# Kernel tuning notes

Hardware: AMD Instinct MI355X
Metric: run time of the kernel (lower is better)

The kernel has to match this reference:

```python
import jax, jax.numpy as jnp
import numpy as np

DIM = 1024
NUM_HEADS = 16
HEAD_DIM = DIM // NUM_HEADS
SCALE = HEAD_DIM ** -0.5
B, N = 2, 2048


def setup_inputs() -> dict:
    key = jax.random.key(0)
    k_x, k_qkv, k_prjw, k_prjb = jax.random.split(key, 4)
    # nn.Linear(dim, 3*dim, bias=False): weight [3*dim, dim]
    s = 1.0 / np.sqrt(DIM)
    return {
        "x": jax.random.normal(k_x, (B, N, DIM), dtype=jnp.float32),
        "w_qkv": jax.random.uniform(k_qkv, (3 * DIM, DIM), jnp.float32, -s, s),
        "w_prj": jax.random.uniform(k_prjw, (DIM, DIM), jnp.float32, -s, s),
        "b_prj": jax.random.uniform(k_prjb, (DIM,), jnp.float32, -s, s),
    }


def reference(x, w_qkv, w_prj, b_prj):
    Bb, Nn, C = x.shape
    qkv = jnp.einsum("bnc,dc->bnd", x, w_qkv)            # [B,N,3C]
    qkv = qkv.reshape(Bb, Nn, 3, NUM_HEADS, HEAD_DIM)
    qkv = jnp.transpose(qkv, (2, 0, 3, 1, 4))            # [3,B,H,N,hd]
    q, k, v = qkv[0], qkv[1], qkv[2]
    attn = jnp.einsum("bhqd,bhkd->bhqk", q, k) * SCALE   # [B,H,N,N]
    attn = jax.nn.softmax(attn, axis=-1)
    out = jnp.einsum("bhqk,bhkd->bhqd", attn, v)         # [B,H,N,hd]
    out = jnp.transpose(out, (0, 2, 1, 3)).reshape(Bb, Nn, C)
    # dropout layers are identity at eval / p=0
    return jnp.einsum("bnc,dc->bnd", out, w_prj) + b_prj
```

## Files before the change

### kernel.cpp

```cpp
#include <hip/hip_runtime.h>

typedef unsigned short u16;
typedef unsigned int u32;
typedef __attribute__((ext_vector_type(8))) short s16x8;
typedef __attribute__((ext_vector_type(4))) short s16x4;
typedef __attribute__((ext_vector_type(4))) float f32x4;

#define DIM    1024
#define NHEADS 16
#define HD     64
#define NSEQ   2048
#define QKVN   3072

__device__ __forceinline__ u16 f2bf(float f) {
  u32 u = __float_as_uint(f);
  u += 0x7FFF + ((u >> 16) & 1);
  return (u16)(u >> 16);
}

__device__ __forceinline__ float vexp2(float x) {
  float r;
  asm volatile("v_exp_f32 %0, %1" : "=v"(r) : "v"(x));
  return r;
}

__device__ __forceinline__ void async16(const u16* g, u16* l) {
  __builtin_amdgcn_global_load_lds(
      (const __attribute__((address_space(1))) unsigned int*)g,
      (__attribute__((address_space(3))) unsigned int*)l, 16, 0, 0);
}

__global__ void cast_all(const float* __restrict__ x, const float* __restrict__ wq,
                         const float* __restrict__ wp, u16* __restrict__ xo,
                         u16* __restrict__ wqo, u16* __restrict__ wpo) {
  int i = blockIdx.x * 256 + threadIdx.x;
  const float4* src; u16* dst; int off;
  if (i < 1048576)      { src = (const float4*)x;  dst = xo;  off = i; }
  else if (i < 1835008) { src = (const float4*)wq; dst = wqo; off = i - 1048576; }
  else                  { src = (const float4*)wp; dst = wpo; off = i - 1835008; }
  float4 f = src[off];
  ushort4 o;
  o.x = f2bf(f.x); o.y = f2bf(f.y); o.z = f2bf(f.z); o.w = f2bf(f.w);
  ((ushort4*)dst)[off] = o;
}

template <bool FINAL>
__global__ __launch_bounds__(256, 3) void gemm_bt(
    const u16* __restrict__ A, const u16* __restrict__ Bw, u16* __restrict__ qkv,
    u16* __restrict__ vt, const float* __restrict__ bias, float* __restrict__ outp) {
  constexpr int K = 1024;
  constexpr int BM = FINAL ? 64 : 128;
  constexpr int MT = FINAL ? 64 : 32;
  constexpr int IT = FINAL ? 2 : 4;
  constexpr int ACALLS = BM / 16;
  constexpr int TCALLS = ACALLS + 8;
  constexpr int PW = TCALLS / 4;
  const int bm = blockIdx.x % MT;
  const int bn = blockIdx.x / MT;
  const int tid = threadIdx.x;
  const int wave = tid >> 6, lane = tid & 63;
  const int q4 = lane >> 4, l15 = lane & 15;
  const int wm = wave >> 1, wn = wave & 1;
  const int m0 = bm * BM, n0 = bn * 128;

  __shared__ alignas(16) u16 lsA[BM * 32];
  __shared__ alignas(16) u16 lsB[128 * 32];

  f32x4 acc[IT][4];
#pragma unroll
  for (int i = 0; i < IT; i++)
#pragma unroll
    for (int j = 0; j < 4; j++) acc[i][j] = (f32x4){0.f, 0.f, 0.f, 0.f};

  for (int k0 = 0; k0 < K; k0 += 32) {
    __syncthreads();
#pragma unroll
    for (int j = 0; j < PW; ++j) {
      int t = wave * PW + j;
      if (t < ACALLS) {
        int lin = t * 64 + lane;
        int r = lin >> 2, c = lin & 3;
        async16(A + (size_t)(m0 + r) * K + k0 + c * 8, lsA + t * 512);
      } else {
        int tb = t - ACALLS;
        int lin = tb * 64 + lane;
        int r = lin >> 2, c = lin & 3;
        async16(Bw + (size_t)(n0 + r) * K + k0 + c * 8, lsB + tb * 512);
      }
    }
    __syncthreads();
    s16x8 af[IT], bfr[4];
#pragma unroll
    for (int i = 0; i < IT; ++i)
      af[i] = *(const s16x8*)(lsA + (wm * (IT * 16) + i * 16 + l15) * 32 + q4 * 8);
#pragma unroll
    for (int j = 0; j < 4; ++j)
      bfr[j] = *(const s16x8*)(lsB + (wn * 64 + j * 16 + l15) * 32 + q4 * 8);
#pragma unroll
    for (int i = 0; i < IT; ++i)
#pragma unroll
      for (int j = 0; j < 4; ++j)
        acc[i][j] = __builtin_amdgcn_mfma_f32_16x16x32_bf16(af[i], bfr[j], acc[i][j], 0, 0, 0);
  }

#pragma unroll
  for (int i = 0; i < IT; i++) {
#pragma unroll
    for (int j = 0; j < 4; j++) {
      int n = n0 + wn * 64 + j * 16 + l15;
      int mb = m0 + wm * (IT * 16) + i * 16 + q4 * 4;
      if (FINAL) {
#pragma unroll
        for (int r = 0; r < 4; r++)
          outp[(size_t)(mb + r) * DIM + n] = acc[i][j][r] + bias[n];
      } else if (n < 2048) {
#pragma unroll
        for (int r = 0; r < 4; r++)
          qkv[(size_t)(mb + r) * QKVN + n] = f2bf(acc[i][j][r]);
      } else {
        int b = mb >> 11, tok = mb & 2047;
        int h = (n >> 6) & 15, hd = n & 63;
        ushort4 pk;
        pk.x = f2bf(acc[i][j][0]); pk.y = f2bf(acc[i][j][1]);
        pk.z = f2bf(acc[i][j][2]); pk.w = f2bf(acc[i][j][3]);
        *(ushort4*)(vt + ((size_t)((b * NHEADS + h) * HD + hd)) * NSEQ + tok) = pk;
      }
    }
  }
}

__global__ __launch_bounds__(256, 2) void attn_kernel(const u16* __restrict__ qkv,
                                                      const u16* __restrict__ vt,
                                                      u16* __restrict__ aout) {
  const int blk = blockIdx.x;
  const int bh = blk & 31, qt = blk >> 5;
  const int b = bh >> 4, h = bh & 15;
  const int tid = threadIdx.x;
  const int wave = tid >> 6, lane = tid & 63;
  const int q4 = lane >> 4, l15 = lane & 15;

  __shared__ alignas(16) u16 lsK[2][64 * 64];
  __shared__ alignas(16) u16 lsV[2][64 * 64];

  const float QSCALE = 0.18033688011112042f;
  s16x8 aq[2][2];
#pragma unroll
  for (int rt = 0; rt < 2; ++rt)
#pragma unroll
    for (int kc = 0; kc < 2; ++kc) {
      int row = b * NSEQ + qt * 128 + wave * 32 + rt * 16 + l15;
      uint4 d = *(const uint4*)(qkv + (size_t)row * QKVN + h * HD + kc * 32 + q4 * 8);
      u32 w[4] = {d.x, d.y, d.z, d.w};
      s16x8 f;
#pragma unroll
      for (int j = 0; j < 8; ++j) {
        u16 u = (u16)(w[j >> 1] >> ((j & 1) * 16));
        float v = __uint_as_float(((u32)u) << 16) * QSCALE;
        f[j] = (short)f2bf(v);
      }
      aq[rt][kc] = f;
    }

  f32x4 o[2][4];
  float lsum[2] = {0.f, 0.f};
#pragma unroll
  for (int rt = 0; rt < 2; ++rt)
#pragma unroll
    for (int ht = 0; ht < 4; ++ht) o[rt][ht] = (f32x4){0.f, 0.f, 0.f, 0.f};

  auto stage = [&](int kt, int buf) {
#pragma unroll
    for (int j = 0; j < 2; ++j) {
      int t = wave * 2 + j;
      int lin = t * 64 + lane;
      int r = lin >> 3, c = (lin & 7) ^ (r & 7);
      async16(qkv + (size_t)(b * NSEQ + kt * 64 + r) * QKVN + DIM + h * HD + c * 8,
              lsK[buf] + t * 512);
      async16(vt + (size_t)(bh * HD + r) * NSEQ + kt * 64 + c * 8,
              lsV[buf] + t * 512);
    }
  };

  stage(0, 0);

  for (int kt = 0; kt < 32; ++kt) {
    const int buf = kt & 1;
    __syncthreads();
    if (kt + 1 < 32) stage(kt + 1, buf ^ 1);

    s16x8 kf[2][4];
#pragma unroll
    for (int kc = 0; kc < 2; ++kc)
#pragma unroll
      for (int ct = 0; ct < 4; ++ct) {
        int r = ct * 16 + l15;
        int c = (kc * 4 + q4) ^ (r & 7);
        kf[kc][ct] = *(const s16x8*)(lsK[buf] + r * 64 + c * 8);
      }
    s16x4 vf[4][4];
#pragma unroll
    for (int ct = 0; ct < 4; ++ct)
#pragma unroll
      for (int ht = 0; ht < 4; ++ht) {
        int row = ht * 16 + l15;
        int g = ct * 2 + (q4 >> 1);
        int p = g ^ (row & 7);
        vf[ct][ht] = *(const s16x4*)(lsV[buf] + row * 64 + p * 8 + (q4 & 1) * 4);
      }

#pragma unroll
    for (int rt = 0; rt < 2; ++rt) {
      f32x4 st[4];
#pragma unroll
      for (int ct = 0; ct < 4; ++ct) st[ct] = (f32x4){0.f, 0.f, 0.f, 0.f};
#pragma unroll
      for (int kc = 0; kc < 2; ++kc)
#pragma unroll
        for (int ct = 0; ct < 4; ++ct)
          st[ct] = __builtin_amdgcn_mfma_f32_16x16x32_bf16(kf[kc][ct], aq[rt][kc], st[ct], 0, 0, 0);

      s16x4 pa[4];
#pragma unroll
      for (int ct = 0; ct < 4; ++ct) {
        u32 u0 = __float_as_uint(vexp2(st[ct][0]));
        u32 u1 = __float_as_uint(vexp2(st[ct][1]));
        u32 u2 = __float_as_uint(vexp2(st[ct][2]));
        u32 u3 = __float_as_uint(vexp2(st[ct][3]));
        lsum[rt] += __uint_as_float(u0 & 0xffff0000u) + __uint_as_float(u1 & 0xffff0000u) +
                    __uint_as_float(u2 & 0xffff0000u) + __uint_as_float(u3 & 0xffff0000u);
        union { u32 w[2]; s16x4 v; } pk;
        pk.w[0] = (u0 >> 16) | (u1 & 0xffff0000u);
        pk.w[1] = (u2 >> 16) | (u3 & 0xffff0000u);
        pa[ct] = pk.v;
      }

#pragma unroll
      for (int ct = 0; ct < 4; ++ct)
#pragma unroll
        for (int ht = 0; ht < 4; ++ht)
          o[rt][ht] = __builtin_amdgcn_mfma_f32_16x16x16bf16_1k(pa[ct], vf[ct][ht], o[rt][ht], 0, 0, 0);
    }
  }

#pragma unroll
  for (int rt = 0; rt < 2; ++rt) {
    lsum[rt] += __shfl_xor(lsum[rt], 16, 64);
    lsum[rt] += __shfl_xor(lsum[rt], 32, 64);
  }

#pragma unroll
  for (int rt = 0; rt < 2; ++rt) {
    float inv[4];
#pragma unroll
    for (int r = 0; r < 4; ++r) inv[r] = 1.0f / __shfl(lsum[rt], q4 * 4 + r, 64);
#pragma unroll
    for (int ht = 0; ht < 4; ++ht)
#pragma unroll
      for (int r = 0; r < 4; ++r) {
        int n = qt * 128 + wave * 32 + rt * 16 + q4 * 4 + r;
        int col = h * HD + ht * 16 + l15;
        aout[(size_t)(b * NSEQ + n) * DIM + col] = f2bf(o[rt][ht][r] * inv[r]);
      }
  }
}

extern "C" void kernel_launch(void* const* d_in, const int* in_sizes, int n_in,
                              void* d_out, int out_size, void* d_ws, size_t ws_size,
                              hipStream_t stream) {
  const float* x     = (const float*)d_in[0];
  const float* w_qkv = (const float*)d_in[1];
  const float* w_prj = (const float*)d_in[2];
  const float* b_prj = (const float*)d_in[3];
  float* out = (float*)d_out;

  char* ws = (char*)d_ws;
  u16* x_bf    = (u16*)(ws);
  u16* wqkv_bf = (u16*)(ws + (size_t)(8u << 20));
  u16* wprj_bf = (u16*)(ws + (size_t)(14u << 20));
  u16* qkv     = (u16*)(ws + (size_t)(16u << 20));
  u16* vt      = (u16*)(ws + (size_t)(40u << 20));
  u16* aout    = (u16*)(ws + (size_t)(48u << 20));

  cast_all<<<8192, 256, 0, stream>>>(x, w_qkv, w_prj, x_bf, wqkv_bf, wprj_bf);
  gemm_bt<false><<<32 * 24, 256, 0, stream>>>(x_bf, wqkv_bf, qkv, vt, nullptr, nullptr);
  attn_kernel<<<512, 256, 0, stream>>>(qkv, vt, aout);
  gemm_bt<true><<<64 * 8, 256, 0, stream>>>(aout, wprj_bf, nullptr, nullptr, b_prj, out);
}
```

Before: 188.0 us.

## Split attention key range across wave groups and merge partial outputs via LDS

The four waves of each attention block are split into two groups. Each group handles half of the key sequence for 64 query rows per wave, so each wave now covers four query tiles instead of two. After the loop, group 1 writes its partial O and row sums to shared memory, and group 0 adds them and normalizes. This raises reuse of each staged K/V tile per wave and halves the loop trip count, at the cost of more registers (doubled accumulators and Q fragments) and an extra LDS reduction at the end. The exp2 inline asm is also replaced by a compiler builtin so the scheduler can see it.

```diff
diff --git a/kernel.cpp b/kernel.cpp
--- a/kernel.cpp
+++ b/kernel.cpp
@@ -19,9 +19,11 @@
 }
 
 __device__ __forceinline__ float vexp2(float x) {
-  float r;
-  asm volatile("v_exp_f32 %0, %1" : "=v"(r) : "v"(x));
-  return r;
+#if __has_builtin(__builtin_amdgcn_exp2f)
+  return __builtin_amdgcn_exp2f(x);
+#else
+  return __expf(x * 0.69314718055994531f);
+#endif
 }
 
 __device__ __forceinline__ void async16(const u16* g, u16* l) {
@@ -137,18 +139,22 @@
   const int b = bh >> 4, h = bh & 15;
   const int tid = threadIdx.x;
   const int wave = tid >> 6, lane = tid & 63;
+  const int g = wave >> 1, wq = wave & 1;
   const int q4 = lane >> 4, l15 = lane & 15;
 
-  __shared__ alignas(16) u16 lsK[2][64 * 64];
-  __shared__ alignas(16) u16 lsV[2][64 * 64];
+  __shared__ alignas(16) u16 smem[32768];
+  u16* lsKb = smem + g * 2 * 4096;
+  u16* lsVb = smem + 16384 + g * 2 * 4096;
+  float* lsO = (float*)smem;
+  float* lsS = lsO + 64 * 132;
 
   const float QSCALE = 0.18033688011112042f;
-  s16x8 aq[2][2];
-#pragma unroll
-  for (int rt = 0; rt < 2; ++rt)
+  s16x8 aq[4][2];
+#pragma unroll
+  for (int rt = 0; rt < 4; ++rt)
 #pragma unroll
     for (int kc = 0; kc < 2; ++kc) {
-      int row = b * NSEQ + qt * 128 + wave * 32 + rt * 16 + l15;
+      int row = b * NSEQ + qt * 128 + wq * 64 + rt * 16 + l15;
       uint4 d = *(const uint4*)(qkv + (size_t)row * QKVN + h * HD + kc * 32 + q4 * 8);
       u32 w[4] = {d.x, d.y, d.z, d.w};
       s16x8 f;
@@ -161,32 +167,35 @@
       aq[rt][kc] = f;
     }
 
-  f32x4 o[2][4];
-  float lsum[2] = {0.f, 0.f};
-#pragma unroll
-  for (int rt = 0; rt < 2; ++rt)
+  f32x4 o[4][4];
+  float lsum[4] = {0.f, 0.f, 0.f, 0.f};
+#pragma unroll
+  for (int rt = 0; rt < 4; ++rt)
 #pragma unroll
     for (int ht = 0; ht < 4; ++ht) o[rt][ht] = (f32x4){0.f, 0.f, 0.f, 0.f};
 
-  auto stage = [&](int kt, int buf) {
-#pragma unroll
-    for (int j = 0; j < 2; ++j) {
-      int t = wave * 2 + j;
+  auto stage = [&](int ktl, int buf) {
+#pragma unroll
+    for (int j = 0; j < 4; ++j) {
+      int t = wq * 4 + j;
       int lin = t * 64 + lane;
       int r = lin >> 3, c = (lin & 7) ^ (r & 7);
-      async16(qkv + (size_t)(b * NSEQ + kt * 64 + r) * QKVN + DIM + h * HD + c * 8,
-              lsK[buf] + t * 512);
-      async16(vt + (size_t)(bh * HD + r) * NSEQ + kt * 64 + c * 8,
-              lsV[buf] + t * 512);
+      int key = g * 1024 + ktl * 64;
+      async16(qkv + (size_t)(b * NSEQ + key + r) * QKVN + DIM + h * HD + c * 8,
+              lsKb + buf * 4096 + t * 512);
+      async16(vt + (size_t)(bh * HD + r) * NSEQ + key + c * 8,
+              lsVb + buf * 4096 + t * 512);
     }
   };
 
   stage(0, 0);
 
-  for (int kt = 0; kt < 32; ++kt) {
+  for (int kt = 0; kt < 16; ++kt) {
     const int buf = kt & 1;
     __syncthreads();
-    if (kt + 1 < 32) stage(kt + 1, buf ^ 1);
+    if (kt + 1 < 16) stage(kt + 1, buf ^ 1);
+    const u16* lsK = lsKb + buf * 4096;
+    const u16* lsV = lsVb + buf * 4096;
 
     s16x8 kf[2][4];
 #pragma unroll
@@ -195,7 +204,7 @@
       for (int ct = 0; ct < 4; ++ct) {
         int r = ct * 16 + l15;
         int c = (kc * 4 + q4) ^ (r & 7);
-        kf[kc][ct] = *(const s16x8*)(lsK[buf] + r * 64 + c * 8);
+        kf[kc][ct] = *(const s16x8*)(lsK + r * 64 + c * 8);
       }
     s16x4 vf[4][4];
 #pragma unroll
@@ -203,13 +212,13 @@
 #pragma unroll
       for (int ht = 0; ht < 4; ++ht) {
         int row = ht * 16 + l15;
-        int g = ct * 2 + (q4 >> 1);
-        int p = g ^ (row & 7);
-        vf[ct][ht] = *(const s16x4*)(lsV[buf] + row * 64 + p * 8 + (q4 & 1) * 4);
-      }
-
-#pragma unroll
-    for (int rt = 0; rt < 2; ++rt) {
+        int gch = ct * 2 + (q4 >> 1);
+        int p = gch ^ (row & 7);
+        vf[ct][ht] = *(const s16x4*)(lsV + row * 64 + p * 8 + (q4 & 1) * 4);
+      }
+
+#pragma unroll
+    for (int rt = 0; rt < 4; ++rt) {
       f32x4 st[4];
 #pragma unroll
       for (int ct = 0; ct < 4; ++ct) st[ct] = (f32x4){0.f, 0.f, 0.f, 0.f};
@@ -243,24 +252,46 @@
   }
 
 #pragma unroll
-  for (int rt = 0; rt < 2; ++rt) {
+  for (int rt = 0; rt < 4; ++rt) {
     lsum[rt] += __shfl_xor(lsum[rt], 16, 64);
     lsum[rt] += __shfl_xor(lsum[rt], 32, 64);
   }
 
-#pragma unroll
-  for (int rt = 0; rt < 2; ++rt) {
-    float inv[4];
-#pragma unroll
-    for (int r = 0; r < 4; ++r) inv[r] = 1.0f / __shfl(lsum[rt], q4 * 4 + r, 64);
-#pragma unroll
-    for (int ht = 0; ht < 4; ++ht)
-#pragma unroll
-      for (int r = 0; r < 4; ++r) {
-        int n = qt * 128 + wave * 32 + rt * 16 + q4 * 4 + r;
-        int col = h * HD + ht * 16 + l15;
-        aout[(size_t)(b * NSEQ + n) * DIM + col] = f2bf(o[rt][ht][r] * inv[r]);
-      }
+  __syncthreads();
+  if (g == 1) {
+#pragma unroll
+    for (int rt = 0; rt < 4; ++rt) {
+#pragma unroll
+      for (int ht = 0; ht < 4; ++ht) {
+        int addr = (ht * 16 + l15) * 132 + wq * 64 + rt * 16 + q4 * 4;
+        *(float4*)(lsO + addr) = (float4){o[rt][ht][0], o[rt][ht][1], o[rt][ht][2], o[rt][ht][3]};
+      }
+      if (q4 == 0) lsS[wq * 64 + rt * 16 + l15] = lsum[rt];
+    }
+  }
+  __syncthreads();
+  if (g == 0) {
+#pragma unroll
+    for (int rt = 0; rt < 4; ++rt) {
+      float4 s2 = *(const float4*)(lsS + wq * 64 + rt * 16 + q4 * 4);
+      float inv[4];
+      inv[0] = 1.0f / (__shfl(lsum[rt], q4 * 4 + 0, 64) + s2.x);
+      inv[1] = 1.0f / (__shfl(lsum[rt], q4 * 4 + 1, 64) + s2.y);
+      inv[2] = 1.0f / (__shfl(lsum[rt], q4 * 4 + 2, 64) + s2.z);
+      inv[3] = 1.0f / (__shfl(lsum[rt], q4 * 4 + 3, 64) + s2.w);
+#pragma unroll
+      for (int ht = 0; ht < 4; ++ht) {
+        float4 o2 = *(const float4*)(lsO + (ht * 16 + l15) * 132 + wq * 64 + rt * 16 + q4 * 4);
+        float v[4] = {o[rt][ht][0] + o2.x, o[rt][ht][1] + o2.y,
+                      o[rt][ht][2] + o2.z, o[rt][ht][3] + o2.w};
+#pragma unroll
+        for (int r = 0; r < 4; ++r) {
+          int n = qt * 128 + wq * 64 + rt * 16 + q4 * 4 + r;
+          int col = h * HD + ht * 16 + l15;
+          aout[(size_t)(b * NSEQ + n) * DIM + col] = f2bf(v[r] * inv[r]);
+        }
+      }
+    }
   }
 }
 
```

Result: faster. 180.2 us (-4.2%).
